# Optimization experiments

Measured on AMD Instinct MI355X. Metric: run time of the kernel, lower is better.

## Reference

```python
import jax, jax.numpy as jnp
import numpy as np

D_MODEL = 512
N_HEADS = 4  # d_model >= 8 -> 4 heads
HEAD_DIM = D_MODEL // N_HEADS
D_FF = 4 * D_MODEL


def setup_inputs() -> dict:
    key = jax.random.key(0)
    ks = jax.random.split(key, 8)
    B, T = 4, 2048
    s = 0.02
    return {
        "x": jax.random.normal(ks[0], (B, T, D_MODEL), dtype=jnp.float32),
        "ln1_g": jnp.ones((D_MODEL,), jnp.float32),
        "ln1_b": jnp.zeros((D_MODEL,), jnp.float32),
        "w_qkv": jax.random.normal(ks[1], (D_MODEL, 3 * D_MODEL), jnp.float32) * s,
        "w_proj": jax.random.normal(ks[2], (D_MODEL, D_MODEL), jnp.float32) * s,
        "ln2_g": jnp.ones((D_MODEL,), jnp.float32),
        "ln2_b": jnp.zeros((D_MODEL,), jnp.float32),
        "w_ff1": jax.random.normal(ks[3], (D_MODEL, D_FF), jnp.float32) * s,
        "w_ff2": jax.random.normal(ks[4], (D_FF, D_MODEL), jnp.float32) * s,
    }


def _layernorm(x, g, b, eps=1e-5):
    mu = jnp.mean(x, axis=-1, keepdims=True)
    var = jnp.var(x, axis=-1, keepdims=True)
    return (x - mu) * jax.lax.rsqrt(var + eps) * g + b


def _attention(x, w_qkv, w_proj):
    B, T, C = x.shape
    qkv = x @ w_qkv  # [B,T,3C]
    q, k, v = jnp.split(qkv, 3, axis=-1)
    # [B,H,T,Dh]
    q = q.reshape(B, T, N_HEADS, HEAD_DIM).transpose(0, 2, 1, 3)
    k = k.reshape(B, T, N_HEADS, HEAD_DIM).transpose(0, 2, 1, 3)
    v = v.reshape(B, T, N_HEADS, HEAD_DIM).transpose(0, 2, 1, 3)
    scale = 1.0 / jnp.sqrt(jnp.asarray(HEAD_DIM, x.dtype))
    scores = jnp.einsum("bhqd,bhkd->bhqk", q, k) * scale
    causal = jnp.tril(jnp.ones((T, T), bool))
    scores = jnp.where(causal, scores, -jnp.inf)
    attn = jax.nn.softmax(scores, axis=-1)
    out = jnp.einsum("bhqk,bhkd->bhqd", attn, v)
    out = out.transpose(0, 2, 1, 3).reshape(B, T, C)
    return out @ w_proj


def reference(x, ln1_g, ln1_b, w_qkv, w_proj, ln2_g, ln2_b, w_ff1, w_ff2):
    x = x + _attention(_layernorm(x, ln1_g, ln1_b), w_qkv, w_proj)
    h = _layernorm(x, ln2_g, ln2_b)
    h = jax.nn.gelu(h @ w_ff1, approximate=False) @ w_ff2
    return x + h
```

## Files before the change

### kernel.cpp

```cpp
#include <hip/hip_runtime.h>
#include <cstdint>

typedef unsigned short u16;
typedef __attribute__((ext_vector_type(8))) short short8;
typedef __attribute__((ext_vector_type(4))) float floatx4;

#define BT    8192
#define TSEQ  2048
#define NBAT  4
#define CMOD  512
#define NH    4
#define HD    128
#define DFF   2048
#define CQKV  1536

__device__ __forceinline__ u16 f2bf(float f) {
  union { float f; uint32_t u; } v; v.f = f;
  uint32_t r = v.u + 0x7FFFu + ((v.u >> 16) & 1u);
  return (u16)(r >> 16);
}
__device__ __forceinline__ float bf2f(u16 u) {
  union { uint32_t u; float f; } v; v.u = ((uint32_t)u) << 16; return v.f;
}
__device__ __forceinline__ float exp2a(float x) {
  float r; asm("v_exp_f32 %0, %1" : "=v"(r) : "v"(x)); return r;
}
__device__ __forceinline__ float rcpa(float x) {
  float r; asm("v_rcp_f32 %0, %1" : "=v"(r) : "v"(x)); return r;
}

typedef __attribute__((address_space(1))) const unsigned int ga_u32;
typedef __attribute__((address_space(3))) unsigned int ls_u32;
__device__ __forceinline__ void glds16(const u16* g, u16* l) {
  __builtin_amdgcn_global_load_lds((ga_u32*)g, (ls_u32*)l, 16, 0, 0);
}

__device__ __forceinline__ void tcast_body(const float* __restrict__ W, u16* __restrict__ Wt,
                                           int K, int N, int bx, int by, int tid,
                                           float (*tile)[33]) {
  int n0 = bx * 32, k0 = by * 32;
  int tx = tid & 31, ty = tid >> 5;
  #pragma unroll
  for (int r = 0; r < 32; r += 8)
    tile[r + ty][tx] = W[(size_t)(k0 + r + ty) * N + n0 + tx];
  __syncthreads();
  #pragma unroll
  for (int r = 0; r < 32; r += 8)
    Wt[(size_t)(n0 + r + ty) * K + k0 + tx] = f2bf(tile[tx][r + ty]);
}

__global__ __launch_bounds__(256) void prep_kernel(
    const float* __restrict__ x, const float* __restrict__ g, const float* __restrict__ b,
    const float* __restrict__ wqkv, const float* __restrict__ wproj,
    const float* __restrict__ wff1, const float* __restrict__ wff2,
    u16* __restrict__ ln_out, u16* __restrict__ wqkvT, u16* __restrict__ wprojT,
    u16* __restrict__ wff1T, u16* __restrict__ wff2T) {
  __shared__ float tile[32][33];
  int bid = blockIdx.x, tid = threadIdx.x;
  if (bid < 768) {
    tcast_body(wqkv, wqkvT, CMOD, CQKV, bid % 48, bid / 48, tid, tile);
  } else if (bid < 1024) {
    int id = bid - 768; tcast_body(wproj, wprojT, CMOD, CMOD, id % 16, id / 16, tid, tile);
  } else if (bid < 2048) {
    int id = bid - 1024; tcast_body(wff1, wff1T, CMOD, DFF, id % 64, id / 64, tid, tile);
  } else if (bid < 3072) {
    int id = bid - 2048; tcast_body(wff2, wff2T, DFF, CMOD, id % 16, id / 16, tid, tile);
  } else {
    int row = (bid - 3072) * 4 + (tid >> 6);
    int lane = tid & 63;
    const float4* xr = (const float4*)(x + (size_t)row * CMOD);
    float4 a = xr[lane], c = xr[lane + 64];
    float s = a.x + a.y + a.z + a.w + c.x + c.y + c.z + c.w;
    float q = a.x*a.x + a.y*a.y + a.z*a.z + a.w*a.w
            + c.x*c.x + c.y*c.y + c.z*c.z + c.w*c.w;
    #pragma unroll
    for (int o = 32; o; o >>= 1) { s += __shfl_xor(s, o); q += __shfl_xor(q, o); }
    float mu = s * (1.0f / CMOD);
    float rstd = rsqrtf(q * (1.0f / CMOD) - mu * mu + 1e-5f);
    const float4* gr = (const float4*)g;
    const float4* br = (const float4*)b;
    float4 g0 = gr[lane], g1 = gr[lane + 64], b0 = br[lane], b1 = br[lane + 64];
    u16* orow = ln_out + (size_t)row * CMOD;
    int i0 = lane * 4, i1 = (lane + 64) * 4;
    orow[i0 + 0] = f2bf((a.x - mu) * rstd * g0.x + b0.x);
    orow[i0 + 1] = f2bf((a.y - mu) * rstd * g0.y + b0.y);
    orow[i0 + 2] = f2bf((a.z - mu) * rstd * g0.z + b0.z);
    orow[i0 + 3] = f2bf((a.w - mu) * rstd * g0.w + b0.w);
    orow[i1 + 0] = f2bf((c.x - mu) * rstd * g1.x + b1.x);
    orow[i1 + 1] = f2bf((c.y - mu) * rstd * g1.y + b1.y);
    orow[i1 + 2] = f2bf((c.z - mu) * rstd * g1.z + b1.z);
    orow[i1 + 3] = f2bf((c.w - mu) * rstd * g1.w + b1.w);
  }
}

__global__ __launch_bounds__(256) void ln_kernel(const float* __restrict__ x,
                                                 const float* __restrict__ g,
                                                 const float* __restrict__ b,
                                                 u16* __restrict__ out) {
  int row = blockIdx.x * 4 + (threadIdx.x >> 6);
  int lane = threadIdx.x & 63;
  const float4* xr = (const float4*)(x + (size_t)row * CMOD);
  float4 a = xr[lane], c = xr[lane + 64];
  float s = a.x + a.y + a.z + a.w + c.x + c.y + c.z + c.w;
  float q = a.x*a.x + a.y*a.y + a.z*a.z + a.w*a.w
          + c.x*c.x + c.y*c.y + c.z*c.z + c.w*c.w;
  #pragma unroll
  for (int o = 32; o; o >>= 1) { s += __shfl_xor(s, o); q += __shfl_xor(q, o); }
  float mu = s * (1.0f / CMOD);
  float rstd = rsqrtf(q * (1.0f / CMOD) - mu * mu + 1e-5f);
  const float4* gr = (const float4*)g;
  const float4* br = (const float4*)b;
  float4 g0 = gr[lane], g1 = gr[lane + 64], b0 = br[lane], b1 = br[lane + 64];
  u16* orow = out + (size_t)row * CMOD;
  int i0 = lane * 4, i1 = (lane + 64) * 4;
  orow[i0 + 0] = f2bf((a.x - mu) * rstd * g0.x + b0.x);
  orow[i0 + 1] = f2bf((a.y - mu) * rstd * g0.y + b0.y);
  orow[i0 + 2] = f2bf((a.z - mu) * rstd * g0.z + b0.z);
  orow[i0 + 3] = f2bf((a.w - mu) * rstd * g0.w + b0.w);
  orow[i1 + 0] = f2bf((c.x - mu) * rstd * g1.x + b1.x);
  orow[i1 + 1] = f2bf((c.y - mu) * rstd * g1.y + b1.y);
  orow[i1 + 2] = f2bf((c.z - mu) * rstd * g1.z + b1.z);
  orow[i1 + 3] = f2bf((c.w - mu) * rstd * g1.w + b1.w);
}

template <int EPI, int TN>
__global__ __launch_bounds__(256, 4) void gemm_kernel(
    const u16* __restrict__ A, const u16* __restrict__ Bt, int K,
    const float* __restrict__ resid, float* __restrict__ outf,
    u16* __restrict__ ob0, u16* __restrict__ ob1, u16* __restrict__ ob2) {
  constexpr int WNF = TN / 32;
  constexpr int NKB = TN / 64;
  __shared__ __align__(16) u16 As[2][128 * 32];
  __shared__ __align__(16) u16 Bs[2][TN * 32];
  int tid = threadIdx.x;
  int lane = tid & 63, wave = tid >> 6;
  int lane16 = lane & 15, quad = lane >> 4;
  int m0 = blockIdx.y * 128, n0 = blockIdx.x * TN;
  int wm = (wave >> 1) * 64, wn = (wave & 1) * (TN / 2);

  floatx4 acc[4][WNF];
  #pragma unroll
  for (int i = 0; i < 4; i++)
    #pragma unroll
    for (int j = 0; j < WNF; j++) acc[i][j] = (floatx4)(0.0f);

  const u16* agp[2]; u16* alp[2][2];
  const u16* bgp[NKB]; u16* blp[NKB][2];
  #pragma unroll
  for (int i = 0; i < 2; i++) {
    int s = i * 256 + tid;
    agp[i] = A + (size_t)(m0 + (s >> 2)) * K + (s & 3) * 8;
    alp[i][0] = &As[0][(i * 256 + wave * 64) * 8];
    alp[i][1] = &As[1][(i * 256 + wave * 64) * 8];
  }
  #pragma unroll
  for (int i = 0; i < NKB; i++) {
    int s = i * 256 + tid;
    bgp[i] = Bt + (size_t)(n0 + (s >> 2)) * K + (s & 3) * 8;
    blp[i][0] = &Bs[0][(i * 256 + wave * 64) * 8];
    blp[i][1] = &Bs[1][(i * 256 + wave * 64) * 8];
  }

  int nk = K >> 5;
  #pragma unroll
  for (int i = 0; i < 2; i++) glds16(agp[i], alp[i][0]);
  #pragma unroll
  for (int i = 0; i < NKB; i++) glds16(bgp[i], blp[i][0]);

  for (int kt = 0; kt < nk; kt++) {
    __syncthreads();
    int buf = kt & 1;
    if (kt + 1 < nk) {
      int k1 = (kt + 1) * 32;
      #pragma unroll
      for (int i = 0; i < 2; i++) glds16(agp[i] + k1, alp[i][buf ^ 1]);
      #pragma unroll
      for (int i = 0; i < NKB; i++) glds16(bgp[i] + k1, blp[i][buf ^ 1]);
    }
    short8 af[4];
    #pragma unroll
    for (int i = 0; i < 4; i++)
      af[i] = *(const short8*)&As[buf][(wm + i * 16 + lane16) * 32 + quad * 8];
    #pragma unroll
    for (int j = 0; j < WNF; j++) {
      short8 bfj = *(const short8*)&Bs[buf][(wn + j * 16 + lane16) * 32 + quad * 8];
      #pragma unroll
      for (int i = 0; i < 4; i++)
        acc[i][j] = __builtin_amdgcn_mfma_f32_16x16x32_bf16(af[i], bfj, acc[i][j], 0, 0, 0);
    }
  }

  #pragma unroll
  for (int i = 0; i < 4; i++) {
    #pragma unroll
    for (int j = 0; j < WNF; j++) {
      #pragma unroll
      for (int r = 0; r < 4; r++) {
        int m = m0 + wm + i * 16 + quad * 4 + r;
        int n = n0 + wn + j * 16 + lane16;
        float v = acc[i][j][r];
        if (EPI == 0) {
          int bb = m >> 11, t = m & 2047;
          int nn = n & 511, which = n >> 9;
          int h = nn >> 7, d = nn & 127;
          size_t bh = (size_t)(bb * NH + h);
          if (which == 0)      ob0[bh * TSEQ * HD + (size_t)t * HD + d] = f2bf(v * 0.12751743f);
          else if (which == 1) ob1[bh * TSEQ * HD + (size_t)t * HD + d] = f2bf(v);
          else                 ob2[bh * HD * TSEQ + (size_t)d * TSEQ + t] = f2bf(v);
        } else if (EPI == 1) {
          size_t idx = (size_t)m * CMOD + n;
          outf[idx] = v + resid[idx];
        } else if (EPI == 2) {
          float ge = 0.5f * v * (1.0f + erff(v * 0.70710678118654752f));
          ob0[(size_t)m * DFF + n] = f2bf(ge);
        } else {
          size_t idx = (size_t)m * CMOD + n;
          outf[idx] = v + resid[idx];
        }
      }
    }
  }
}

__global__ __launch_bounds__(256) void attn_kernel(const u16* __restrict__ qb,
                                                   const u16* __restrict__ kb,
                                                   const u16* __restrict__ vtb,
                                                   u16* __restrict__ po,
                                                   float* __restrict__ pl) {
  __shared__ __align__(16) u16 Ks[2][32 * 128];
  __shared__ __align__(16) u16 Vs[2][128 * 32];
  __shared__ __align__(16) uint32_t Ps[4 * 16 * 20];
  int tid = threadIdx.x, wave = tid >> 6, lane = tid & 63;
  int lane16 = lane & 15, quad = lane >> 4;
  int bh = blockIdx.x;
  int cid = 79 - (int)blockIdx.y;
  int qt, c;
  if (cid < 8)       { qt = cid;                    c = 0; }
  else if (cid < 24) { qt = 8 + ((cid - 8) >> 1);   c = (cid - 8) & 1; }
  else if (cid < 48) { qt = 16 + (cid - 24) / 3;    c = (cid - 24) % 3; }
  else               { qt = 24 + ((cid - 48) >> 2); c = (cid - 48) & 3; }

  int q0w = qt * 64 + wave * 16;
  const u16* Q  = qb  + (size_t)bh * TSEQ * HD;
  const u16* Kg = kb  + (size_t)bh * TSEQ * HD;
  const u16* Vg = vtb + (size_t)bh * HD * TSEQ;

  short8 aq[4];
  {
    int qrow = q0w + lane16;
    #pragma unroll
    for (int cc = 0; cc < 4; cc++)
      aq[cc] = *(const short8*)&Q[(size_t)qrow * HD + cc * 32 + quad * 8];
  }

  const u16* kgp[2]; const u16* vgp[2];
  u16* klp[2][2]; u16* vlp[2][2];
  #pragma unroll
  for (int i = 0; i < 2; i++) {
    int s = wave * 128 + i * 64 + lane;
    int r = s >> 4, cp = s & 15, cc = cp ^ (r & 7);
    kgp[i] = Kg + (size_t)r * HD + cc * 8;
    int d = s >> 2, cv = (s & 3) ^ ((d >> 1) & 3);
    vgp[i] = Vg + (size_t)d * TSEQ + cv * 8;
    #pragma unroll
    for (int bfr = 0; bfr < 2; bfr++) {
      klp[i][bfr] = &Ks[bfr][(wave * 128 + i * 64) * 8];
      vlp[i][bfr] = &Vs[bfr][(wave * 128 + i * 64) * 8];
    }
  }

  int ktw   = (q0w >> 5) + 1;
  int ktblk = qt * 2 + 2;
  int kt0   = c * 16;
  int kend  = min(kt0 + 16, ktblk);

  floatx4 o[8];
  #pragma unroll
  for (int j = 0; j < 8; j++) o[j] = (floatx4)(0.0f);
  floatx4 ol = (floatx4)(0.0f);

  short8 ones;
  #pragma unroll
  for (int e = 0; e < 8; e++) ones[e] = (short)0x3F80;

  uint32_t* Pw = &Ps[wave * 320];
  int swl = lane16 & 7;
  int cvr = quad ^ ((lane16 >> 1) & 3);

  {
    int ko = kt0 * 32;
    #pragma unroll
    for (int i = 0; i < 2; i++) {
      glds16(kgp[i] + (size_t)ko * HD, klp[i][kt0 & 1]);
      glds16(vgp[i] + ko, vlp[i][kt0 & 1]);
    }
  }

  for (int kt = kt0; kt < kend; kt++) {
    __syncthreads();
    int buf = kt & 1;
    if (kt + 1 < kend) {
      int ko = (kt + 1) * 32;
      #pragma unroll
      for (int i = 0; i < 2; i++) {
        glds16(kgp[i] + (size_t)ko * HD, klp[i][buf ^ 1]);
        glds16(vgp[i] + ko, vlp[i][buf ^ 1]);
      }
    }
    if (kt >= ktw) continue;

    floatx4 st0 = (floatx4)(0.0f), st1 = (floatx4)(0.0f);
    #pragma unroll
    for (int cc = 0; cc < 4; cc++) {
      short8 kf0 = *(const short8*)&Ks[buf][(lane16 * 16 + ((cc * 4 + quad) ^ swl)) * 8];
      short8 kf1 = *(const short8*)&Ks[buf][((16 + lane16) * 16 + ((cc * 4 + quad) ^ swl)) * 8];
      st0 = __builtin_amdgcn_mfma_f32_16x16x32_bf16(aq[cc], kf0, st0, 0, 0, 0);
      st1 = __builtin_amdgcn_mfma_f32_16x16x32_bf16(aq[cc], kf1, st1, 0, 0, 0);
    }
    short8 vf[8];
    #pragma unroll
    for (int j = 0; j < 8; j++)
      vf[j] = *(const short8*)&Vs[buf][((j * 16 + lane16) * 4 + cvr) * 8];

    int kg0 = kt * 32 + lane16;
    #pragma unroll
    for (int r = 0; r < 4; r++) {
      int qr = q0w + quad * 4 + r;
      float p0 = exp2a(st0[r]);
      float p1 = exp2a(st1[r]);
      if (kg0 > qr) p0 = 0.0f;
      if (kg0 + 16 > qr) p1 = 0.0f;
      Pw[(quad * 4 + r) * 20 + lane16] =
          __builtin_amdgcn_perm(__float_as_uint(p1), __float_as_uint(p0), 0x07060302u);
    }
    asm volatile("s_waitcnt lgkmcnt(0)" ::: "memory");

    union { uint32_t u[4]; short8 s; } pf;
    {
      const uint32_t* prow = &Pw[lane16 * 20 + (quad & 1) * 8];
      uint32_t d0 = prow[0], d1 = prow[1], d2 = prow[2], d3 = prow[3];
      uint32_t d4 = prow[4], d5 = prow[5], d6 = prow[6], d7 = prow[7];
      uint32_t sel = (quad >> 1) ? 0x07060302u : 0x05040100u;
      pf.u[0] = __builtin_amdgcn_perm(d1, d0, sel);
      pf.u[1] = __builtin_amdgcn_perm(d3, d2, sel);
      pf.u[2] = __builtin_amdgcn_perm(d5, d4, sel);
      pf.u[3] = __builtin_amdgcn_perm(d7, d6, sel);
    }
    #pragma unroll
    for (int j = 0; j < 8; j++)
      o[j] = __builtin_amdgcn_mfma_f32_16x16x32_bf16(pf.s, vf[j], o[j], 0, 0, 0);
    ol = __builtin_amdgcn_mfma_f32_16x16x32_bf16(pf.s, ones, ol, 0, 0, 0);
  }

  int slot = (bh * 32 + qt) * 4 + c;
  u16* pob = po + (size_t)slot * 8192;
  #pragma unroll
  for (int r = 0; r < 4; r++) {
    int qr = wave * 16 + quad * 4 + r;
    #pragma unroll
    for (int j = 0; j < 8; j++)
      pob[qr * 128 + j * 16 + lane16] = f2bf(o[j][r]);
    if (lane16 == 0) pl[slot * 64 + qr] = ol[r];
  }
}

__global__ __launch_bounds__(256) void reduce_kernel(const u16* __restrict__ po,
                                                     const float* __restrict__ pl,
                                                     u16* __restrict__ attn) {
  int bh = blockIdx.x >> 5, qt = blockIdx.x & 31;
  int tid = threadIdx.x;
  int nch = (2 * qt + 17) >> 4;
  int qrow = tid >> 2;
  int d0 = (tid & 3) * 32;
  float acc[32];
  #pragma unroll
  for (int i = 0; i < 32; i++) acc[i] = 0.0f;
  float l = 0.0f;
  int slot0 = (bh * 32 + qt) * 4;
  for (int c = 0; c < nch; c++) {
    int slot = slot0 + c;
    l += pl[slot * 64 + qrow];
    const short8* p = (const short8*)(po + (size_t)slot * 8192 + qrow * 128 + d0);
    #pragma unroll
    for (int v = 0; v < 4; v++) {
      short8 pk = p[v];
      #pragma unroll
      for (int e = 0; e < 8; e++) acc[v * 8 + e] += bf2f((u16)pk[e]);
    }
  }
  float inv = rcpa(l);
  int b = bh >> 2, h = bh & 3, t = qt * 64 + qrow;
  u16* orow = attn + ((size_t)(b * TSEQ + t)) * CMOD + h * HD + d0;
  #pragma unroll
  for (int v = 0; v < 4; v++) {
    short8 ov;
    #pragma unroll
    for (int e = 0; e < 8; e++) ov[e] = (short)f2bf(acc[v * 8 + e] * inv);
    *(short8*)(orow + v * 8) = ov;
  }
}

extern "C" void kernel_launch(void* const* d_in, const int* in_sizes, int n_in,
                              void* d_out, int out_size, void* d_ws, size_t ws_size,
                              hipStream_t stream) {
  const float* x     = (const float*)d_in[0];
  const float* ln1g  = (const float*)d_in[1];
  const float* ln1b  = (const float*)d_in[2];
  const float* wqkv  = (const float*)d_in[3];
  const float* wproj = (const float*)d_in[4];
  const float* ln2g  = (const float*)d_in[5];
  const float* ln2b  = (const float*)d_in[6];
  const float* wff1  = (const float*)d_in[7];
  const float* wff2  = (const float*)d_in[8];
  float* out = (float*)d_out;
  char* ws = (char*)d_ws;

  u16* wt_qkv  = (u16*)(ws);
  u16* wt_proj = (u16*)(ws + 1572864);
  u16* wt_ff1  = (u16*)(ws + 2097152);
  u16* wt_ff2  = (u16*)(ws + 4194304);
  u16* ln_buf  = (u16*)(ws + 6291456);
  u16* q_buf   = (u16*)(ws + 14680064);
  u16* k_buf   = (u16*)(ws + 23068672);
  u16* vt_buf  = (u16*)(ws + 31457280);
  u16* attn    = (u16*)(ws + 39845888);
  float* x2    = (float*)(ws + 48234496);
  u16* h1      = (u16*)(ws + 65011712);
  u16* po      = (u16*)(ws + 48234496);
  float* pl    = (float*)(ws + 81788928);

  dim3 blk(256);
  prep_kernel<<<dim3(5120), blk, 0, stream>>>(x, ln1g, ln1b, wqkv, wproj, wff1, wff2,
                                              ln_buf, wt_qkv, wt_proj, wt_ff1, wt_ff2);

  gemm_kernel<0, 128><<<dim3(CQKV / 128, BT / 128), blk, 0, stream>>>(
      ln_buf, wt_qkv, CMOD, nullptr, nullptr, q_buf, k_buf, vt_buf);

  attn_kernel<<<dim3(NBAT * NH, 80), blk, 0, stream>>>(q_buf, k_buf, vt_buf, po, pl);

  reduce_kernel<<<dim3(512), blk, 0, stream>>>(po, pl, attn);

  gemm_kernel<1, 64><<<dim3(CMOD / 64, BT / 128), blk, 0, stream>>>(
      attn, wt_proj, CMOD, x, x2, nullptr, nullptr, nullptr);

  ln_kernel<<<dim3(BT / 4), blk, 0, stream>>>(x2, ln2g, ln2b, ln_buf);

  gemm_kernel<2, 128><<<dim3(DFF / 128, BT / 128), blk, 0, stream>>>(
      ln_buf, wt_ff1, CMOD, nullptr, nullptr, h1, nullptr, nullptr);

  gemm_kernel<3, 64><<<dim3(CMOD / 64, BT / 128), blk, 0, stream>>>(
      h1, wt_ff2, DFF, x2, out, nullptr, nullptr, nullptr);
}
```

Measured before the change: 269.0 us.

## Double attention query tile per wave to reuse K/V LDS loads

Each wave now processes 32 query rows (two 16-row MFMA tiles) instead of 16, so every block covers 128 queries and each K/V tile loaded into LDS feeds twice as many MFMAs. The grid shrinks from 80 to 40 chunks per head, and the partial-output layout and reduce kernel are rescaled to match. This halves K/V global traffic and LDS fragment reads per query, at the cost of more accumulator registers (possibly lower occupancy), fewer blocks, and a coarser causal split that wastes more masked work.

```diff
diff --git a/kernel.cpp b/kernel.cpp
--- a/kernel.cpp
+++ b/kernel.cpp
@@ -229,28 +229,27 @@
                                                    float* __restrict__ pl) {
   __shared__ __align__(16) u16 Ks[2][32 * 128];
   __shared__ __align__(16) u16 Vs[2][128 * 32];
-  __shared__ __align__(16) uint32_t Ps[4 * 16 * 20];
+  __shared__ __align__(16) uint32_t Ps[4 * 32 * 20];
   int tid = threadIdx.x, wave = tid >> 6, lane = tid & 63;
   int lane16 = lane & 15, quad = lane >> 4;
   int bh = blockIdx.x;
-  int cid = 79 - (int)blockIdx.y;
-  int qt, c;
-  if (cid < 8)       { qt = cid;                    c = 0; }
-  else if (cid < 24) { qt = 8 + ((cid - 8) >> 1);   c = (cid - 8) & 1; }
-  else if (cid < 48) { qt = 16 + (cid - 24) / 3;    c = (cid - 24) % 3; }
-  else               { qt = 24 + ((cid - 48) >> 2); c = (cid - 48) & 3; }
-
-  int q0w = qt * 64 + wave * 16;
+  int cid = (int)blockIdx.y;
+  int qq, c;
+  if (cid < 16)      { qq = 15 - (cid >> 2);           c = cid & 3; }
+  else if (cid < 28) { int t = cid - 16; qq = 11 - t / 3; c = t % 3; }
+  else if (cid < 36) { int t = cid - 28; qq = 7 - (t >> 1); c = t & 1; }
+  else               { qq = 39 - cid;                  c = 0; }
+
+  int q0w = qq * 128 + wave * 32;
   const u16* Q  = qb  + (size_t)bh * TSEQ * HD;
   const u16* Kg = kb  + (size_t)bh * TSEQ * HD;
   const u16* Vg = vtb + (size_t)bh * HD * TSEQ;
 
-  short8 aq[4];
-  {
-    int qrow = q0w + lane16;
-    #pragma unroll
-    for (int cc = 0; cc < 4; cc++)
-      aq[cc] = *(const short8*)&Q[(size_t)qrow * HD + cc * 32 + quad * 8];
+  short8 aqA[4], aqB[4];
+  #pragma unroll
+  for (int cc = 0; cc < 4; cc++) {
+    aqA[cc] = *(const short8*)&Q[(size_t)(q0w + lane16) * HD + cc * 32 + quad * 8];
+    aqB[cc] = *(const short8*)&Q[(size_t)(q0w + 16 + lane16) * HD + cc * 32 + quad * 8];
   }
 
   const u16* kgp[2]; const u16* vgp[2];
@@ -269,21 +268,21 @@
     }
   }
 
-  int ktw   = (q0w >> 5) + 1;
-  int ktblk = qt * 2 + 2;
+  int ktw   = 4 * qq + wave + 1;
+  int ktblk = 4 * qq + 4;
   int kt0   = c * 16;
   int kend  = min(kt0 + 16, ktblk);
 
-  floatx4 o[8];
-  #pragma unroll
-  for (int j = 0; j < 8; j++) o[j] = (floatx4)(0.0f);
-  floatx4 ol = (floatx4)(0.0f);
+  floatx4 oA[8], oB[8];
+  #pragma unroll
+  for (int j = 0; j < 8; j++) { oA[j] = (floatx4)(0.0f); oB[j] = (floatx4)(0.0f); }
+  floatx4 olA = (floatx4)(0.0f), olB = (floatx4)(0.0f);
 
   short8 ones;
   #pragma unroll
   for (int e = 0; e < 8; e++) ones[e] = (short)0x3F80;
 
-  uint32_t* Pw = &Ps[wave * 320];
+  uint32_t* Pw = &Ps[wave * 640];
   int swl = lane16 & 7;
   int cvr = quad ^ ((lane16 >> 1) & 3);
 
@@ -309,13 +308,16 @@
     }
     if (kt >= ktw) continue;
 
-    floatx4 st0 = (floatx4)(0.0f), st1 = (floatx4)(0.0f);
+    floatx4 sA0 = (floatx4)(0.0f), sA1 = (floatx4)(0.0f);
+    floatx4 sB0 = (floatx4)(0.0f), sB1 = (floatx4)(0.0f);
     #pragma unroll
     for (int cc = 0; cc < 4; cc++) {
       short8 kf0 = *(const short8*)&Ks[buf][(lane16 * 16 + ((cc * 4 + quad) ^ swl)) * 8];
       short8 kf1 = *(const short8*)&Ks[buf][((16 + lane16) * 16 + ((cc * 4 + quad) ^ swl)) * 8];
-      st0 = __builtin_amdgcn_mfma_f32_16x16x32_bf16(aq[cc], kf0, st0, 0, 0, 0);
-      st1 = __builtin_amdgcn_mfma_f32_16x16x32_bf16(aq[cc], kf1, st1, 0, 0, 0);
+      sA0 = __builtin_amdgcn_mfma_f32_16x16x32_bf16(aqA[cc], kf0, sA0, 0, 0, 0);
+      sA1 = __builtin_amdgcn_mfma_f32_16x16x32_bf16(aqA[cc], kf1, sA1, 0, 0, 0);
+      sB0 = __builtin_amdgcn_mfma_f32_16x16x32_bf16(aqB[cc], kf0, sB0, 0, 0, 0);
+      sB1 = __builtin_amdgcn_mfma_f32_16x16x32_bf16(aqB[cc], kf1, sB1, 0, 0, 0);
     }
     short8 vf[8];
     #pragma unroll
@@ -325,74 +327,91 @@
     int kg0 = kt * 32 + lane16;
     #pragma unroll
     for (int r = 0; r < 4; r++) {
-      int qr = q0w + quad * 4 + r;
-      float p0 = exp2a(st0[r]);
-      float p1 = exp2a(st1[r]);
-      if (kg0 > qr) p0 = 0.0f;
-      if (kg0 + 16 > qr) p1 = 0.0f;
+      int qrA = q0w + quad * 4 + r, qrB = qrA + 16;
+      float pA0 = exp2a(sA0[r]);
+      float pA1 = exp2a(sA1[r]);
+      float pB0 = exp2a(sB0[r]);
+      float pB1 = exp2a(sB1[r]);
+      if (kg0 > qrA) pA0 = 0.0f;
+      if (kg0 + 16 > qrA) pA1 = 0.0f;
+      if (kg0 > qrB) pB0 = 0.0f;
+      if (kg0 + 16 > qrB) pB1 = 0.0f;
       Pw[(quad * 4 + r) * 20 + lane16] =
-          __builtin_amdgcn_perm(__float_as_uint(p1), __float_as_uint(p0), 0x07060302u);
+          __builtin_amdgcn_perm(__float_as_uint(pA1), __float_as_uint(pA0), 0x07060302u);
+      Pw[(16 + quad * 4 + r) * 20 + lane16] =
+          __builtin_amdgcn_perm(__float_as_uint(pB1), __float_as_uint(pB0), 0x07060302u);
     }
     asm volatile("s_waitcnt lgkmcnt(0)" ::: "memory");
 
-    union { uint32_t u[4]; short8 s; } pf;
+    union { uint32_t u[4]; short8 s; } pfA, pfB;
     {
-      const uint32_t* prow = &Pw[lane16 * 20 + (quad & 1) * 8];
-      uint32_t d0 = prow[0], d1 = prow[1], d2 = prow[2], d3 = prow[3];
-      uint32_t d4 = prow[4], d5 = prow[5], d6 = prow[6], d7 = prow[7];
       uint32_t sel = (quad >> 1) ? 0x07060302u : 0x05040100u;
-      pf.u[0] = __builtin_amdgcn_perm(d1, d0, sel);
-      pf.u[1] = __builtin_amdgcn_perm(d3, d2, sel);
-      pf.u[2] = __builtin_amdgcn_perm(d5, d4, sel);
-      pf.u[3] = __builtin_amdgcn_perm(d7, d6, sel);
-    }
-    #pragma unroll
-    for (int j = 0; j < 8; j++)
-      o[j] = __builtin_amdgcn_mfma_f32_16x16x32_bf16(pf.s, vf[j], o[j], 0, 0, 0);
-    ol = __builtin_amdgcn_mfma_f32_16x16x32_bf16(pf.s, ones, ol, 0, 0, 0);
-  }
-
-  int slot = (bh * 32 + qt) * 4 + c;
-  u16* pob = po + (size_t)slot * 8192;
+      const uint32_t* pra = &Pw[lane16 * 20 + (quad & 1) * 8];
+      pfA.u[0] = __builtin_amdgcn_perm(pra[1], pra[0], sel);
+      pfA.u[1] = __builtin_amdgcn_perm(pra[3], pra[2], sel);
+      pfA.u[2] = __builtin_amdgcn_perm(pra[5], pra[4], sel);
+      pfA.u[3] = __builtin_amdgcn_perm(pra[7], pra[6], sel);
+      const uint32_t* prb = &Pw[(16 + lane16) * 20 + (quad & 1) * 8];
+      pfB.u[0] = __builtin_amdgcn_perm(prb[1], prb[0], sel);
+      pfB.u[1] = __builtin_amdgcn_perm(prb[3], prb[2], sel);
+      pfB.u[2] = __builtin_amdgcn_perm(prb[5], prb[4], sel);
+      pfB.u[3] = __builtin_amdgcn_perm(prb[7], prb[6], sel);
+    }
+    #pragma unroll
+    for (int j = 0; j < 8; j++) {
+      oA[j] = __builtin_amdgcn_mfma_f32_16x16x32_bf16(pfA.s, vf[j], oA[j], 0, 0, 0);
+      oB[j] = __builtin_amdgcn_mfma_f32_16x16x32_bf16(pfB.s, vf[j], oB[j], 0, 0, 0);
+    }
+    olA = __builtin_amdgcn_mfma_f32_16x16x32_bf16(pfA.s, ones, olA, 0, 0, 0);
+    olB = __builtin_amdgcn_mfma_f32_16x16x32_bf16(pfB.s, ones, olB, 0, 0, 0);
+  }
+
+  int slot = (bh * 16 + qq) * 4 + c;
+  u16* pob = po + (size_t)slot * 16384;
   #pragma unroll
   for (int r = 0; r < 4; r++) {
-    int qr = wave * 16 + quad * 4 + r;
-    #pragma unroll
-    for (int j = 0; j < 8; j++)
-      pob[qr * 128 + j * 16 + lane16] = f2bf(o[j][r]);
-    if (lane16 == 0) pl[slot * 64 + qr] = ol[r];
+    int qrA = wave * 32 + quad * 4 + r, qrB = qrA + 16;
+    #pragma unroll
+    for (int j = 0; j < 8; j++) {
+      pob[qrA * 128 + j * 16 + lane16] = f2bf(oA[j][r]);
+      pob[qrB * 128 + j * 16 + lane16] = f2bf(oB[j][r]);
+    }
+    if (lane16 == 0) {
+      pl[slot * 128 + qrA] = olA[r];
+      pl[slot * 128 + qrB] = olB[r];
+    }
   }
 }
 
 __global__ __launch_bounds__(256) void reduce_kernel(const u16* __restrict__ po,
                                                      const float* __restrict__ pl,
                                                      u16* __restrict__ attn) {
-  int bh = blockIdx.x >> 5, qt = blockIdx.x & 31;
+  int bh = blockIdx.x >> 4, qq = blockIdx.x & 15;
   int tid = threadIdx.x;
-  int nch = (2 * qt + 17) >> 4;
-  int qrow = tid >> 2;
-  int d0 = (tid & 3) * 32;
-  float acc[32];
-  #pragma unroll
-  for (int i = 0; i < 32; i++) acc[i] = 0.0f;
+  int nch = (4 * qq + 19) >> 4;
+  int qrow = tid >> 1;
+  int d0 = (tid & 1) * 64;
+  float acc[64];
+  #pragma unroll
+  for (int i = 0; i < 64; i++) acc[i] = 0.0f;
   float l = 0.0f;
-  int slot0 = (bh * 32 + qt) * 4;
+  int slot0 = (bh * 16 + qq) * 4;
   for (int c = 0; c < nch; c++) {
     int slot = slot0 + c;
-    l += pl[slot * 64 + qrow];
-    const short8* p = (const short8*)(po + (size_t)slot * 8192 + qrow * 128 + d0);
-    #pragma unroll
-    for (int v = 0; v < 4; v++) {
+    l += pl[slot * 128 + qrow];
+    const short8* p = (const short8*)(po + (size_t)slot * 16384 + qrow * 128 + d0);
+    #pragma unroll
+    for (int v = 0; v < 8; v++) {
       short8 pk = p[v];
       #pragma unroll
       for (int e = 0; e < 8; e++) acc[v * 8 + e] += bf2f((u16)pk[e]);
     }
   }
   float inv = rcpa(l);
-  int b = bh >> 2, h = bh & 3, t = qt * 64 + qrow;
+  int b = bh >> 2, h = bh & 3, t = qq * 128 + qrow;
   u16* orow = attn + ((size_t)(b * TSEQ + t)) * CMOD + h * HD + d0;
   #pragma unroll
-  for (int v = 0; v < 4; v++) {
+  for (int v = 0; v < 8; v++) {
     short8 ov;
     #pragma unroll
     for (int e = 0; e < 8; e++) ov[e] = (short)f2bf(acc[v * 8 + e] * inv);
@@ -436,9 +455,9 @@
   gemm_kernel<0, 128><<<dim3(CQKV / 128, BT / 128), blk, 0, stream>>>(
       ln_buf, wt_qkv, CMOD, nullptr, nullptr, q_buf, k_buf, vt_buf);
 
-  attn_kernel<<<dim3(NBAT * NH, 80), blk, 0, stream>>>(q_buf, k_buf, vt_buf, po, pl);
-
-  reduce_kernel<<<dim3(512), blk, 0, stream>>>(po, pl, attn);
+  attn_kernel<<<dim3(NBAT * NH, 40), blk, 0, stream>>>(q_buf, k_buf, vt_buf, po, pl);
+
+  reduce_kernel<<<dim3(256), blk, 0, stream>>>(po, pl, attn);
 
   gemm_kernel<1, 64><<<dim3(CMOD / 64, BT / 128), blk, 0, stream>>>(
       attn, wt_proj, CMOD, x, x2, nullptr, nullptr, nullptr);
```

Measured after the change: 275.7 us. +2.5%, slower.
